# Kernel tuning notes

Measured on AMD Instinct MI355X. Metric: run time of the kernel, lower is better.

Reference implementation:

```python
import jax, jax.numpy as jnp
import numpy as np

D_MODEL = 1024
N_HEADS = 16
ALPHA = 0.7
C_PARAM = 5
CUTOFF = C_PARAM // 2 + 1  # 3
LN_EPS = 1e-12
B, S = 4, 2048


def setup_inputs() -> dict:
    key = jax.random.key(0)
    ks = jax.random.split(key, 10)
    d = D_MODEL
    scale = 1.0 / np.sqrt(d)
    return {
        "input_tensor": jax.random.normal(ks[0], (B, S, d), dtype=jnp.float32),
        "attention_mask": jnp.ones((1, 1, S, S), dtype=jnp.int32),
        "sqrt_beta": jax.random.normal(ks[1], (1, 1, d), dtype=jnp.float32),
        "ln_gamma": jnp.ones((d,), dtype=jnp.float32),
        "ln_beta": jnp.zeros((d,), dtype=jnp.float32),
        "q_w": jax.random.normal(ks[2], (d, d), dtype=jnp.float32) * scale,
        "q_b": jnp.zeros((d,), dtype=jnp.float32),
        "k_w": jax.random.normal(ks[3], (d, d), dtype=jnp.float32) * scale,
        "k_b": jnp.zeros((d,), dtype=jnp.float32),
        "v_w": jax.random.normal(ks[4], (d, d), dtype=jnp.float32) * scale,
        "v_b": jnp.zeros((d,), dtype=jnp.float32),
    }


def _layer_norm(x, g, b):
    mu = jnp.mean(x, axis=-1, keepdims=True)
    var = jnp.mean(jnp.square(x - mu), axis=-1, keepdims=True)
    return (x - mu) * jax.lax.rsqrt(var + LN_EPS) * g + b


def bsarec_layer(x, mask, sqrt_beta, ln_gamma, ln_beta, q_w, q_b, k_w, k_b, v_w, v_b):
    batch, seq_len, hidden = x.shape
    # ---- FrequencyLayer (DSP branch) ----
    xf = jnp.fft.rfft(x, axis=1, norm='ortho')                 # [B, S//2+1, D]
    freq = jnp.arange(xf.shape[1])[None, :, None]
    low_pass = jnp.fft.irfft(jnp.where(freq < CUTOFF, xf, 0.0), n=seq_len, axis=1, norm='ortho')
    high_pass = x - low_pass
    seq_fft = low_pass + jnp.square(sqrt_beta) * high_pass
    dsp = _layer_norm(seq_fft + x, ln_gamma, ln_beta)          # dropout=0 -> identity
    # ---- MultiHeadAttention (GSP branch) ----
    h, d_k = N_HEADS, hidden // N_HEADS
    def split(t):  # [B,S,D] -> [B,H,S,d_k]
        return t.reshape(batch, seq_len, h, d_k).transpose(0, 2, 1, 3)
    q = split(x @ q_w.T + q_b)
    k = split(x @ k_w.T + k_b)
    v = split(x @ v_w.T + v_b)
    scores = jnp.einsum('bhsd,bhtd->bhst', q, k) / jnp.sqrt(jnp.float32(d_k))
    scores = jnp.where(mask == 0, -jnp.inf, scores)
    scores = scores - jnp.max(scores)                           # global max, as in source
    p = jax.nn.softmax(scores, axis=-1)
    p = jnp.where(jnp.isnan(p), 0.0, p)
    out = jnp.einsum('bhst,bhtd->bhsd', p, v)
    gsp = out.transpose(0, 2, 1, 3).reshape(batch, seq_len, hidden)
    return ALPHA * dsp + (1.0 - ALPHA) * gsp


def reference(input_tensor, attention_mask, sqrt_beta, ln_gamma, ln_beta, q_w, q_b, k_w, k_b, v_w, v_b):
    return bsarec_layer(input_tensor, attention_mask, sqrt_beta, ln_gamma, ln_beta,
                        q_w, q_b, k_w, k_b, v_w, v_b)
```

## Files before the change

kernel.cpp:

```cpp
#include <hip/hip_runtime.h>

#define S_LEN 2048
#define DM 1024
#define NB 4
#define NROWS (NB * S_LEN)
#define NHEADS 16
#define DK 64

typedef __bf16 bf16x8 __attribute__((ext_vector_type(8)));
typedef __bf16 bf16x2 __attribute__((ext_vector_type(2)));
typedef float f32x4 __attribute__((ext_vector_type(4)));
typedef float f32x2 __attribute__((ext_vector_type(2)));

struct __align__(8) us4 { unsigned short x, y, z, w; };

__device__ __forceinline__ unsigned cvt2(float a, float b) {
    f32x2 t; t.x = a; t.y = b;
    bf16x2 h = __builtin_convertvector(t, bf16x2);
    return __builtin_bit_cast(unsigned, h);
}
__device__ __forceinline__ unsigned short f2bf(float f) {
    __bf16 h = (__bf16)f;
    return __builtin_bit_cast(unsigned short, h);
}

__device__ __forceinline__ void gl2lds16(const void* g, void* l) {
    __builtin_amdgcn_global_load_lds(
        (const __attribute__((address_space(1))) unsigned int*)g,
        (__attribute__((address_space(3))) unsigned int*)l, 16, 0, 0);
}

__device__ __forceinline__ void bar_lgkm() {
    __builtin_amdgcn_s_waitcnt(0xC07F);
    __builtin_amdgcn_s_barrier();
}

__global__ __launch_bounds__(256) void prep(
    const float* __restrict__ x, float* __restrict__ coef,
    unsigned short* __restrict__ xbf, const float* __restrict__ qw,
    const float* __restrict__ kw, const float* __restrict__ vw,
    unsigned short* __restrict__ wbf) {
    int bx = blockIdx.x;
    if (bx >= 512) {
        int idx = ((bx - 512) * 256 + threadIdx.x) * 2;
        int which = idx >> 20, off = idx & 0xFFFFF;
        const float* src = (which == 0) ? qw : ((which == 1) ? kw : vw);
        float2 v = *(const float2*)(&src[off]);
        *(unsigned*)(&wbf[idx]) = cvt2(v.x, v.y);
        return;
    }
    int b = bx >> 7, dc = (bx >> 5) & 3, tc = bx & 31;
    int d = dc * 256 + threadIdx.x;
    __shared__ float tw[4][64];
    if (threadIdx.x < 64) {
        const float omega = 6.283185307179586476925f / (float)S_LEN;
        float sn, cs;
        __sincosf(omega * (float)(tc * 64 + threadIdx.x), &sn, &cs);
        tw[0][threadIdx.x] = sn;
        tw[1][threadIdx.x] = cs;
        tw[2][threadIdx.x] = 2.f * sn * cs;
        tw[3][threadIdx.x] = cs * cs - sn * sn;
    }
    __syncthreads();
    float c0 = 0.f, c1 = 0.f, s1 = 0.f, c2 = 0.f, s2 = 0.f;
    for (int i = 0; i < 64; ++i) {
        int t = tc * 64 + i;
        long idx = (long)(b * S_LEN + t) * DM + d;
        float v = x[idx];
        xbf[idx] = f2bf(v);
        c0 += v;
        c1 += v * tw[1][i];
        s1 += v * tw[0][i];
        c2 += v * tw[3][i];
        s2 += v * tw[2][i];
    }
    int base = b * DM + d;
    atomicAdd(&coef[0 * 4096 + base], c0);
    atomicAdd(&coef[1 * 4096 + base], c1);
    atomicAdd(&coef[2 * 4096 + base], s1);
    atomicAdd(&coef[3 * 4096 + base], c2);
    atomicAdd(&coef[4 * 4096 + base], s2);
}

__global__ __launch_bounds__(256) void dsp_ln(
    const float* __restrict__ x, const float* __restrict__ coef,
    const float* __restrict__ sqrt_beta, const float* __restrict__ gamma,
    const float* __restrict__ beta, const unsigned short* __restrict__ Og,
    float* __restrict__ out) {
    int row = blockIdx.x;
    int b = row >> 11, t = row & (S_LEN - 1);
    int tid = threadIdx.x, lane = tid & 63, wave = tid >> 6;
    const float omega = 6.283185307179586476925f / (float)S_LEN;
    float sn, cs;
    __sincosf(omega * (float)t, &sn, &cs);
    float c2t = cs * cs - sn * sn, s2t = 2.f * sn * cs;
    int d0 = tid * 4;
    long base = (long)row * DM;
    float4 xv = *(const float4*)(&x[base + d0]);
    int cb = b * DM + d0;
    float4 C0 = *(const float4*)(&coef[0 * 4096 + cb]);
    float4 C1 = *(const float4*)(&coef[1 * 4096 + cb]);
    float4 S1 = *(const float4*)(&coef[2 * 4096 + cb]);
    float4 C2 = *(const float4*)(&coef[3 * 4096 + cb]);
    float4 S2 = *(const float4*)(&coef[4 * 4096 + cb]);
    float4 sb = *(const float4*)(&sqrt_beta[d0]);
    const float inv_s = 1.0f / (float)S_LEN;
    float y[4];
#pragma unroll
    for (int i = 0; i < 4; ++i) {
        float c0 = (&C0.x)[i], c1 = (&C1.x)[i], s1 = (&S1.x)[i],
              c2 = (&C2.x)[i], s2 = (&S2.x)[i];
        float lp = (c0 + 2.f * (c1 * cs + s1 * sn) + 2.f * (c2 * c2t + s2 * s2t)) * inv_s;
        float xx = (&xv.x)[i];
        float b2 = (&sb.x)[i];
        b2 = b2 * b2;
        y[i] = xx + lp + b2 * (xx - lp);
    }
    float ssum = y[0] + y[1] + y[2] + y[3];
    float ssq = y[0] * y[0] + y[1] * y[1] + y[2] * y[2] + y[3] * y[3];
#pragma unroll
    for (int m = 1; m < 64; m <<= 1) {
        ssum += __shfl_xor(ssum, m, 64);
        ssq += __shfl_xor(ssq, m, 64);
    }
    __shared__ float red[8];
    if (lane == 0) { red[wave] = ssum; red[4 + wave] = ssq; }
    __syncthreads();
    float S = red[0] + red[1] + red[2] + red[3];
    float SQ = red[4] + red[5] + red[6] + red[7];
    float mu = S * (1.0f / DM);
    float var = SQ * (1.0f / DM) - mu * mu;
    float rstd = rsqrtf(var + 1e-12f);
    float4 g = *(const float4*)(&gamma[d0]);
    float4 be = *(const float4*)(&beta[d0]);
    us4 gv = *(const us4*)(&Og[((long)((b << 4) + (d0 >> 6)) * S_LEN + t) * DK + (d0 & 63)]);
    const unsigned short* gp = (const unsigned short*)&gv;
    float4 o;
#pragma unroll
    for (int i = 0; i < 4; ++i)
        (&o.x)[i] = 0.7f * ((y[i] - mu) * rstd * (&g.x)[i] + (&be.x)[i]) +
                    0.3f * __uint_as_float((unsigned)gp[i] << 16);
    *(float4*)(&out[base + d0]) = o;
}

__global__ __launch_bounds__(256) void gemm_qkv(
    const unsigned short* __restrict__ A, const unsigned short* __restrict__ W,
    const float* __restrict__ qb, const float* __restrict__ kb,
    const float* __restrict__ vb, unsigned short* __restrict__ Qo,
    unsigned short* __restrict__ Ko, unsigned short* __restrict__ Vt_g) {
    const int m0 = blockIdx.y * 128;
    const int n0g = blockIdx.x * 128;
    const int which = n0g >> 10;
    const int n0 = n0g & 1023;
    const int tid = threadIdx.x;
    const int lane = tid & 63, wave = tid >> 6;
    const int wm = wave >> 1, wn = wave & 1;
    const int r = lane & 15, q = lane >> 4;
    __shared__ __align__(16) unsigned short Sm[8192];
    unsigned short* As = Sm;
    unsigned short* Bs = Sm + 4096;
    const int lrow = lane >> 2;
    const int lch = (lane & 3) * 8;
    f32x4 acc[4][4] = {};
    for (int k0 = 0; k0 < DM; k0 += 32) {
        __syncthreads();
#pragma unroll
        for (int e = 0; e < 2; ++e) {
            int blk = e * 4 + wave;
            int row = blk * 16 + lrow;
            gl2lds16(&A[(long)(m0 + row) * DM + k0 + lch], &As[blk * 512 + lane * 8]);
            gl2lds16(&W[(long)(n0g + row) * DM + k0 + lch], &Bs[blk * 512 + lane * 8]);
        }
        __syncthreads();
        bf16x8 af[4], bfr[4];
#pragma unroll
        for (int i = 0; i < 4; ++i) {
            af[i] = *(const bf16x8*)(&As[(wm * 64 + i * 16 + r) * 32 + q * 8]);
            bfr[i] = *(const bf16x8*)(&Bs[(wn * 64 + i * 16 + r) * 32 + q * 8]);
        }
#pragma unroll
        for (int mi = 0; mi < 4; ++mi)
#pragma unroll
            for (int ni = 0; ni < 4; ++ni)
                acc[mi][ni] = __builtin_amdgcn_mfma_f32_16x16x32_bf16(
                    af[mi], bfr[ni], acc[mi][ni], 0, 0, 0);
    }
    const float* bias = (which == 0) ? qb : ((which == 1) ? kb : vb);
    if (which < 2) {
        unsigned short* Out = (which == 0) ? Qo : Ko;
#pragma unroll
        for (int p = 0; p < 4; ++p) {
            __syncthreads();
            if (wm == (p >> 1)) {
#pragma unroll
                for (int mi2 = 0; mi2 < 2; ++mi2) {
                    int mi = (p & 1) * 2 + mi2;
                    int rowL = mi2 * 16 + q * 4;
#pragma unroll
                    for (int ni = 0; ni < 4; ++ni) {
                        int col = wn * 64 + ni * 16 + r;
                        float bv = bias[n0 + col];
#pragma unroll
                        for (int reg = 0; reg < 4; ++reg)
                            Sm[(rowL + reg) * 134 + col] = f2bf(acc[mi][ni][reg] + bv);
                    }
                }
            }
            __syncthreads();
            int rowL = wave * 8 + (lane >> 3);
            int cc = (lane & 7) * 16;
            uint4 w0 = *(const uint4*)(&Sm[rowL * 134 + cc]);
            uint4 w1 = *(const uint4*)(&Sm[rowL * 134 + cc + 8]);
            long gb = (long)(m0 + p * 32 + rowL) * DM + n0 + cc;
            *(uint4*)(&Out[gb]) = w0;
            *(uint4*)(&Out[gb + 8]) = w1;
        }
    } else {
        const int bb = m0 >> 11, sg = m0 & (S_LEN - 1);
#pragma unroll
        for (int p = 0; p < 4; ++p) {
            __syncthreads();
            if (wn == (p >> 1)) {
#pragma unroll
                for (int ni2 = 0; ni2 < 2; ++ni2) {
                    int ni = (p & 1) * 2 + ni2;
                    int colL = ni2 * 16 + r;
                    float bv = bias[n0 + p * 32 + colL];
#pragma unroll
                    for (int mi = 0; mi < 4; ++mi) {
                        int s = wm * 64 + mi * 16 + q * 4;
                        *(unsigned*)(&Sm[colL * 134 + s]) =
                            cvt2(acc[mi][ni][0] + bv, acc[mi][ni][1] + bv);
                        *(unsigned*)(&Sm[colL * 134 + s + 2]) =
                            cvt2(acc[mi][ni][2] + bv, acc[mi][ni][3] + bv);
                    }
                }
            }
            __syncthreads();
            int colL = wave * 8 + (lane >> 3);
            int sc = (lane & 7) * 16;
            uint4 w0 = *(const uint4*)(&Sm[colL * 134 + sc]);
            uint4 w1 = *(const uint4*)(&Sm[colL * 134 + sc + 8]);
            long gb = ((long)bb * DM + n0 + p * 32 + colL) * S_LEN + sg + sc;
            *(uint4*)(&Vt_g[gb]) = w0;
            *(uint4*)(&Vt_g[gb + 8]) = w1;
        }
    }
}

__global__ __launch_bounds__(256, 2) void attn(
    const unsigned short* __restrict__ Q, const unsigned short* __restrict__ K,
    const unsigned short* __restrict__ Vt_g, unsigned short* __restrict__ Og) {
    int bx = blockIdx.x;
    int bh = bx & 63, qt = bx >> 6;
    int b = bh >> 4, h = bh & 15;
    const int tid = threadIdx.x, lane = tid & 63, wave = tid >> 6;
    const int r = lane & 15, q = lane >> 4;
    const int hc = h * DK;
    const int q0 = qt * 256 + wave * 64;
    bf16x8 aq[4][2];
#pragma unroll
    for (int mt = 0; mt < 4; ++mt) {
        long rowQ = (long)(b * S_LEN + q0 + mt * 16 + r) * DM + hc;
        aq[mt][0] = *(const bf16x8*)(&Q[rowQ + q * 8]);
        aq[mt][1] = *(const bf16x8*)(&Q[rowQ + 32 + q * 8]);
    }
    __shared__ __align__(16) unsigned short Ks[2][64 * 72];
    __shared__ __align__(16) unsigned short Vt[2][64 * 72];
    __shared__ __align__(16) unsigned short Ps[4 * 64 * 40];
    __shared__ float denL[4 * 64];
    f32x4 accO[4][4] = {};
    float den[4] = {};
    const int srow = tid >> 3;
    const int sch = (tid & 7) * 8;
    const long kbase = (long)b * S_LEN * DM + hc + sch;
    const long vbase = ((long)bh * DK + srow) * S_LEN + sch;
    int4 kreg[2], vreg[2];
#pragma unroll
    for (int e = 0; e < 2; ++e) {
        kreg[e] = *(const int4*)(&K[kbase + (long)(e * 32 + srow) * DM]);
        vreg[e] = *(const int4*)(&Vt_g[vbase + (long)e * 32 * S_LEN]);
    }
#pragma unroll
    for (int e = 0; e < 2; ++e) {
        int rw = e * 32 + srow;
        *(int4*)(&Ks[0][rw * 72 + sch]) = kreg[e];
        *(int4*)(&Vt[0][rw * 72 + sch]) = vreg[e];
    }
    bar_lgkm();
    for (int t = 0; t < 32; ++t) {
        const unsigned short* Kc = Ks[t & 1];
        const unsigned short* Vc = Vt[t & 1];
        if (t < 31) {
            int jn = (t + 1) * 64;
#pragma unroll
            for (int e = 0; e < 2; ++e) {
                kreg[e] = *(const int4*)(&K[kbase + (long)(jn + e * 32 + srow) * DM]);
                vreg[e] = *(const int4*)(&Vt_g[vbase + (long)e * 32 * S_LEN + jn]);
            }
        }
#pragma unroll
        for (int c = 0; c < 2; ++c) {
#pragma unroll
            for (int jt2 = 0; jt2 < 2; ++jt2) {
                int jt = c * 2 + jt2;
                bf16x8 ak0 = *(const bf16x8*)(&Kc[(jt * 16 + r) * 72 + q * 8]);
                bf16x8 ak1 = *(const bf16x8*)(&Kc[(jt * 16 + r) * 72 + 32 + q * 8]);
#pragma unroll
                for (int mt = 0; mt < 4; ++mt) {
                    f32x4 s = {};
                    s = __builtin_amdgcn_mfma_f32_16x16x32_bf16(ak0, aq[mt][0], s, 0, 0, 0);
                    s = __builtin_amdgcn_mfma_f32_16x16x32_bf16(ak1, aq[mt][1], s, 0, 0, 0);
                    float p0 = __expf(s[0] * 0.125f);
                    float p1 = __expf(s[1] * 0.125f);
                    float p2 = __expf(s[2] * 0.125f);
                    float p3 = __expf(s[3] * 0.125f);
                    den[mt] += (p0 + p1) + (p2 + p3);
                    us4 pk;
                    pk.x = f2bf(p0); pk.y = f2bf(p1);
                    pk.z = f2bf(p2); pk.w = f2bf(p3);
                    *(us4*)(&Ps[(wave * 64 + mt * 16 + r) * 40 + jt2 * 16 + q * 4]) = pk;
                }
            }
            bf16x8 ap[4];
#pragma unroll
            for (int mt = 0; mt < 4; ++mt)
                ap[mt] = *(const bf16x8*)(&Ps[(wave * 64 + mt * 16 + r) * 40 + q * 8]);
#pragma unroll
            for (int dt = 0; dt < 4; ++dt) {
                bf16x8 bv = *(const bf16x8*)(&Vc[(dt * 16 + r) * 72 + c * 32 + q * 8]);
#pragma unroll
                for (int mt = 0; mt < 4; ++mt)
                    accO[mt][dt] = __builtin_amdgcn_mfma_f32_16x16x32_bf16(
                        ap[mt], bv, accO[mt][dt], 0, 0, 0);
            }
        }
        if (t < 31) {
#pragma unroll
            for (int e = 0; e < 2; ++e) {
                int rw = e * 32 + srow;
                *(int4*)(&Ks[(t + 1) & 1][rw * 72 + sch]) = kreg[e];
                *(int4*)(&Vt[(t + 1) & 1][rw * 72 + sch]) = vreg[e];
            }
        }
        bar_lgkm();
    }
#pragma unroll
    for (int mt = 0; mt < 4; ++mt) {
        float d = den[mt];
        d += __shfl_xor(d, 16, 64);
        d += __shfl_xor(d, 32, 64);
        if (q == 0) denL[wave * 64 + mt * 16 + r] = d;
    }
#pragma unroll
    for (int mt = 0; mt < 4; ++mt) {
        float4 dv = *(const float4*)(&denL[wave * 64 + mt * 16 + q * 4]);
        float rs[4];
#pragma unroll
        for (int reg = 0; reg < 4; ++reg) rs[reg] = 1.0f / (&dv.x)[reg];
        long obase = (long)bh * S_LEN + q0 + mt * 16 + q * 4;
#pragma unroll
        for (int dt = 0; dt < 4; ++dt) {
            int col = dt * 16 + r;
#pragma unroll
            for (int reg = 0; reg < 4; ++reg)
                Og[(obase + reg) * DK + col] = f2bf(accO[mt][dt][reg] * rs[reg]);
        }
    }
}

extern "C" void kernel_launch(void* const* d_in, const int* in_sizes, int n_in,
                              void* d_out, int out_size, void* d_ws, size_t ws_size,
                              hipStream_t stream) {
    const float* x = (const float*)d_in[0];
    const float* sqrt_beta = (const float*)d_in[2];
    const float* gamma = (const float*)d_in[3];
    const float* beta = (const float*)d_in[4];
    const float* qw = (const float*)d_in[5];
    const float* qb = (const float*)d_in[6];
    const float* kw = (const float*)d_in[7];
    const float* kb = (const float*)d_in[8];
    const float* vw = (const float*)d_in[9];
    const float* vb = (const float*)d_in[10];
    float* out = (float*)d_out;

    char* ws = (char*)d_ws;
    float* coef = (float*)ws;
    unsigned short* xbf = (unsigned short*)(ws + 81920);
    unsigned short* wbf = (unsigned short*)(ws + 81920 + 16777216);
    unsigned short* Qb = (unsigned short*)(ws + 81920 + 16777216 + 6291456);
    unsigned short* Kb = Qb + (long)NROWS * DM;
    unsigned short* Vt_g = Kb + (long)NROWS * DM;
    unsigned short* Og = xbf;

    hipMemsetAsync(coef, 0, 5 * 4096 * sizeof(float), stream);
    prep<<<6656, 256, 0, stream>>>(x, coef, xbf, qw, kw, vw, wbf);
    dim3 ggrid(3 * DM / 128, NROWS / 128);
    gemm_qkv<<<ggrid, 256, 0, stream>>>(xbf, wbf, qb, kb, vb, Qb, Kb, Vt_g);
    attn<<<NB * NHEADS * (S_LEN / 256), 256, 0, stream>>>(Qb, Kb, Vt_g, Og);
    dsp_ln<<<NROWS, 256, 0, stream>>>(x, coef, sqrt_beta, gamma, beta, Og, out);
}
```

Baseline: 304.9 us.

## Restructure attention: register-resident P, async LDS loads, exp2 prescaled Q, smaller tiles

The attention kernel now keeps softmax probabilities in registers and feeds them straight into the PV MFMA, which removes the Ps shared-memory round trip. K and V tiles are loaded with global_load_lds directly into swizzled, unpadded LDS. The softmax scale and log2(e) are folded into Q in the GEMM epilogue so exp2 can replace expf. The query tile per block is halved to 128 rows, which doubles the grid and raises the occupancy target to 3 blocks per CU. In exchange the kernel relies on subtle swizzle index math and on the bf16 rounding of the scaled Q.

```diff
diff --git a/kernel.cpp b/kernel.cpp
--- a/kernel.cpp
+++ b/kernel.cpp
@@ -11,6 +11,7 @@
 typedef __bf16 bf16x2 __attribute__((ext_vector_type(2)));
 typedef float f32x4 __attribute__((ext_vector_type(4)));
 typedef float f32x2 __attribute__((ext_vector_type(2)));
+typedef unsigned u32x4 __attribute__((ext_vector_type(4)));
 
 struct __align__(8) us4 { unsigned short x, y, z, w; };
 
@@ -30,10 +31,11 @@
         (__attribute__((address_space(3))) unsigned int*)l, 16, 0, 0);
 }
 
-__device__ __forceinline__ void bar_lgkm() {
-    __builtin_amdgcn_s_waitcnt(0xC07F);
-    __builtin_amdgcn_s_barrier();
-}
+#if __has_builtin(__builtin_amdgcn_exp2f)
+#define EXP2F(x) __builtin_amdgcn_exp2f(x)
+#else
+#define EXP2F(x) exp2f(x)
+#endif
 
 __global__ __launch_bounds__(256) void prep(
     const float* __restrict__ x, float* __restrict__ coef,
@@ -187,6 +189,7 @@
     }
     const float* bias = (which == 0) ? qb : ((which == 1) ? kb : vb);
     if (which < 2) {
+        const float qs = (which == 0) ? 0.18033688011112042f : 1.0f;
         unsigned short* Out = (which == 0) ? Qo : Ko;
 #pragma unroll
         for (int p = 0; p < 4; ++p) {
@@ -202,7 +205,7 @@
                         float bv = bias[n0 + col];
 #pragma unroll
                         for (int reg = 0; reg < 4; ++reg)
-                            Sm[(rowL + reg) * 134 + col] = f2bf(acc[mi][ni][reg] + bv);
+                            Sm[(rowL + reg) * 134 + col] = f2bf((acc[mi][ni][reg] + bv) * qs);
                     }
                 }
             }
@@ -248,7 +251,7 @@
     }
 }
 
-__global__ __launch_bounds__(256, 2) void attn(
+__global__ __launch_bounds__(256, 3) void attn(
     const unsigned short* __restrict__ Q, const unsigned short* __restrict__ K,
     const unsigned short* __restrict__ Vt_g, unsigned short* __restrict__ Og) {
     int bx = blockIdx.x;
@@ -257,104 +260,113 @@
     const int tid = threadIdx.x, lane = tid & 63, wave = tid >> 6;
     const int r = lane & 15, q = lane >> 4;
     const int hc = h * DK;
-    const int q0 = qt * 256 + wave * 64;
-    bf16x8 aq[4][2];
-#pragma unroll
-    for (int mt = 0; mt < 4; ++mt) {
+    const int q0 = qt * 128 + wave * 32;
+
+    bf16x8 aq[2][2];
+#pragma unroll
+    for (int mt = 0; mt < 2; ++mt) {
         long rowQ = (long)(b * S_LEN + q0 + mt * 16 + r) * DM + hc;
         aq[mt][0] = *(const bf16x8*)(&Q[rowQ + q * 8]);
         aq[mt][1] = *(const bf16x8*)(&Q[rowQ + 32 + q * 8]);
     }
-    __shared__ __align__(16) unsigned short Ks[2][64 * 72];
-    __shared__ __align__(16) unsigned short Vt[2][64 * 72];
-    __shared__ __align__(16) unsigned short Ps[4 * 64 * 40];
-    __shared__ float denL[4 * 64];
-    f32x4 accO[4][4] = {};
-    float den[4] = {};
-    const int srow = tid >> 3;
-    const int sch = (tid & 7) * 8;
-    const long kbase = (long)b * S_LEN * DM + hc + sch;
-    const long vbase = ((long)bh * DK + srow) * S_LEN + sch;
-    int4 kreg[2], vreg[2];
-#pragma unroll
-    for (int e = 0; e < 2; ++e) {
-        kreg[e] = *(const int4*)(&K[kbase + (long)(e * 32 + srow) * DM]);
-        vreg[e] = *(const int4*)(&Vt_g[vbase + (long)e * 32 * S_LEN]);
-    }
-#pragma unroll
-    for (int e = 0; e < 2; ++e) {
-        int rw = e * 32 + srow;
-        *(int4*)(&Ks[0][rw * 72 + sch]) = kreg[e];
-        *(int4*)(&Vt[0][rw * 72 + sch]) = vreg[e];
-    }
-    bar_lgkm();
+
+    __shared__ __align__(16) unsigned short Ks[2][4096];
+    __shared__ __align__(16) unsigned short Vt[2][4096];
+    __shared__ float denL[128];
+
+    f32x4 accO[2][4] = {};
+    float den[2] = {};
+
+    const int lr = lane >> 3, lc = lane & 7;
+    const int cw0 = wave * 2, cw1 = cw0 + 1;
+    const int ld0 = cw0 * 512, ld1 = cw1 * 512;
+    const int row0 = cw0 * 8 + lr, row1 = cw1 * 8 + lr;
+    const int f0 = (lr + 2 * (cw0 & 3)) & 7;
+    const int f1 = (lr + 2 * (cw1 & 3)) & 7;
+    const int cg0 = (lc - f0) & 7, cg1 = (lc - f1) & 7;
+    const unsigned short* kp0 = K + (long)(b * S_LEN + row0) * DM + hc + cg0 * 8;
+    const unsigned short* kp1 = K + (long)(b * S_LEN + row1) * DM + hc + cg1 * 8;
+    const unsigned short* vp0 = Vt_g + (long)(bh * 64 + row0) * S_LEN + cg0 * 8;
+    const unsigned short* vp1 = Vt_g + (long)(bh * 64 + row1) * S_LEN + cg1 * 8;
+
+    const int lo = r & 3, hi = r >> 2;
+    const int abase = (hi * 8 + lo) * 64;
+    const int e0 = (q + lo + 2 * hi) & 7;
+    const int ca = e0 * 8;
+    const int cb2 = ((e0 + 4) & 7) * 8;
+    const int fv = ((r & 7) + 2 * (r >> 3)) & 7;
+    const int vca = ((q + fv) & 7) * 8;
+    const int vcb = ((q + fv + 4) & 7) * 8;
+
+    gl2lds16(kp0, &Ks[0][ld0 + lane * 8]);
+    gl2lds16(kp1, &Ks[0][ld1 + lane * 8]);
+    gl2lds16(vp0, &Vt[0][ld0 + lane * 8]);
+    gl2lds16(vp1, &Vt[0][ld1 + lane * 8]);
+    kp0 += 64 * DM; kp1 += 64 * DM; vp0 += 64; vp1 += 64;
+    asm volatile("s_waitcnt vmcnt(0)" ::: "memory");
+    __builtin_amdgcn_s_barrier();
+
     for (int t = 0; t < 32; ++t) {
-        const unsigned short* Kc = Ks[t & 1];
-        const unsigned short* Vc = Vt[t & 1];
+        const int cur = t & 1;
         if (t < 31) {
-            int jn = (t + 1) * 64;
-#pragma unroll
-            for (int e = 0; e < 2; ++e) {
-                kreg[e] = *(const int4*)(&K[kbase + (long)(jn + e * 32 + srow) * DM]);
-                vreg[e] = *(const int4*)(&Vt_g[vbase + (long)e * 32 * S_LEN + jn]);
+            const int nb = cur ^ 1;
+            gl2lds16(kp0, &Ks[nb][ld0 + lane * 8]);
+            gl2lds16(kp1, &Ks[nb][ld1 + lane * 8]);
+            gl2lds16(vp0, &Vt[nb][ld0 + lane * 8]);
+            gl2lds16(vp1, &Vt[nb][ld1 + lane * 8]);
+            kp0 += 64 * DM; kp1 += 64 * DM; vp0 += 64; vp1 += 64;
+        }
+        const unsigned short* Kc = Ks[cur];
+        const unsigned short* Vc = Vt[cur];
+#pragma unroll
+        for (int c = 0; c < 2; ++c) {
+            const int cb64 = c * 2048;
+            bf16x8 ak00 = *(const bf16x8*)(&Kc[cb64 + abase + ca]);
+            bf16x8 ak01 = *(const bf16x8*)(&Kc[cb64 + abase + cb2]);
+            bf16x8 ak10 = *(const bf16x8*)(&Kc[cb64 + 256 + abase + cb2]);
+            bf16x8 ak11 = *(const bf16x8*)(&Kc[cb64 + 256 + abase + ca]);
+            const int va = c ? vcb : vca;
+            const int vb2 = c ? vca : vcb;
+            bf16x8 bv[4];
+            bv[0] = *(const bf16x8*)(&Vc[(0 * 16 + r) * 64 + va]);
+            bv[1] = *(const bf16x8*)(&Vc[(1 * 16 + r) * 64 + vb2]);
+            bv[2] = *(const bf16x8*)(&Vc[(2 * 16 + r) * 64 + va]);
+            bv[3] = *(const bf16x8*)(&Vc[(3 * 16 + r) * 64 + vb2]);
+#pragma unroll
+            for (int mt = 0; mt < 2; ++mt) {
+                f32x4 sa = {}, sb = {};
+                sa = __builtin_amdgcn_mfma_f32_16x16x32_bf16(ak00, aq[mt][0], sa, 0, 0, 0);
+                sa = __builtin_amdgcn_mfma_f32_16x16x32_bf16(ak01, aq[mt][1], sa, 0, 0, 0);
+                sb = __builtin_amdgcn_mfma_f32_16x16x32_bf16(ak10, aq[mt][0], sb, 0, 0, 0);
+                sb = __builtin_amdgcn_mfma_f32_16x16x32_bf16(ak11, aq[mt][1], sb, 0, 0, 0);
+                float p0 = EXP2F(sa[0]), p1 = EXP2F(sa[1]);
+                float p2 = EXP2F(sa[2]), p3 = EXP2F(sa[3]);
+                float p4 = EXP2F(sb[0]), p5 = EXP2F(sb[1]);
+                float p6 = EXP2F(sb[2]), p7 = EXP2F(sb[3]);
+                den[mt] += ((p0 + p1) + (p2 + p3)) + ((p4 + p5) + (p6 + p7));
+                u32x4 wv;
+                wv.x = cvt2(p0, p1); wv.y = cvt2(p2, p3);
+                wv.z = cvt2(p4, p5); wv.w = cvt2(p6, p7);
+                bf16x8 ap = __builtin_bit_cast(bf16x8, wv);
+#pragma unroll
+                for (int dt = 0; dt < 4; ++dt)
+                    accO[mt][dt] = __builtin_amdgcn_mfma_f32_16x16x32_bf16(
+                        ap, bv[dt], accO[mt][dt], 0, 0, 0);
             }
         }
-#pragma unroll
-        for (int c = 0; c < 2; ++c) {
-#pragma unroll
-            for (int jt2 = 0; jt2 < 2; ++jt2) {
-                int jt = c * 2 + jt2;
-                bf16x8 ak0 = *(const bf16x8*)(&Kc[(jt * 16 + r) * 72 + q * 8]);
-                bf16x8 ak1 = *(const bf16x8*)(&Kc[(jt * 16 + r) * 72 + 32 + q * 8]);
-#pragma unroll
-                for (int mt = 0; mt < 4; ++mt) {
-                    f32x4 s = {};
-                    s = __builtin_amdgcn_mfma_f32_16x16x32_bf16(ak0, aq[mt][0], s, 0, 0, 0);
-                    s = __builtin_amdgcn_mfma_f32_16x16x32_bf16(ak1, aq[mt][1], s, 0, 0, 0);
-                    float p0 = __expf(s[0] * 0.125f);
-                    float p1 = __expf(s[1] * 0.125f);
-                    float p2 = __expf(s[2] * 0.125f);
-                    float p3 = __expf(s[3] * 0.125f);
-                    den[mt] += (p0 + p1) + (p2 + p3);
-                    us4 pk;
-                    pk.x = f2bf(p0); pk.y = f2bf(p1);
-                    pk.z = f2bf(p2); pk.w = f2bf(p3);
-                    *(us4*)(&Ps[(wave * 64 + mt * 16 + r) * 40 + jt2 * 16 + q * 4]) = pk;
-                }
-            }
-            bf16x8 ap[4];
-#pragma unroll
-            for (int mt = 0; mt < 4; ++mt)
-                ap[mt] = *(const bf16x8*)(&Ps[(wave * 64 + mt * 16 + r) * 40 + q * 8]);
-#pragma unroll
-            for (int dt = 0; dt < 4; ++dt) {
-                bf16x8 bv = *(const bf16x8*)(&Vc[(dt * 16 + r) * 72 + c * 32 + q * 8]);
-#pragma unroll
-                for (int mt = 0; mt < 4; ++mt)
-                    accO[mt][dt] = __builtin_amdgcn_mfma_f32_16x16x32_bf16(
-                        ap[mt], bv, accO[mt][dt], 0, 0, 0);
-            }
-        }
-        if (t < 31) {
-#pragma unroll
-            for (int e = 0; e < 2; ++e) {
-                int rw = e * 32 + srow;
-                *(int4*)(&Ks[(t + 1) & 1][rw * 72 + sch]) = kreg[e];
-                *(int4*)(&Vt[(t + 1) & 1][rw * 72 + sch]) = vreg[e];
-            }
-        }
-        bar_lgkm();
-    }
-#pragma unroll
-    for (int mt = 0; mt < 4; ++mt) {
+        asm volatile("s_waitcnt vmcnt(0)" ::: "memory");
+        __builtin_amdgcn_s_barrier();
+    }
+#pragma unroll
+    for (int mt = 0; mt < 2; ++mt) {
         float d = den[mt];
         d += __shfl_xor(d, 16, 64);
         d += __shfl_xor(d, 32, 64);
-        if (q == 0) denL[wave * 64 + mt * 16 + r] = d;
-    }
-#pragma unroll
-    for (int mt = 0; mt < 4; ++mt) {
-        float4 dv = *(const float4*)(&denL[wave * 64 + mt * 16 + q * 4]);
+        if (q == 0) denL[wave * 32 + mt * 16 + r] = d;
+    }
+#pragma unroll
+    for (int mt = 0; mt < 2; ++mt) {
+        float4 dv = *(const float4*)(&denL[wave * 32 + mt * 16 + q * 4]);
         float rs[4];
 #pragma unroll
         for (int reg = 0; reg < 4; ++reg) rs[reg] = 1.0f / (&dv.x)[reg];
@@ -397,6 +409,6 @@
     prep<<<6656, 256, 0, stream>>>(x, coef, xbf, qw, kw, vw, wbf);
     dim3 ggrid(3 * DM / 128, NROWS / 128);
     gemm_qkv<<<ggrid, 256, 0, stream>>>(xbf, wbf, qb, kb, vb, Qb, Kb, Vt_g);
-    attn<<<NB * NHEADS * (S_LEN / 256), 256, 0, stream>>>(Qb, Kb, Vt_g, Og);
+    attn<<<NB * NHEADS * (S_LEN / 128), 256, 0, stream>>>(Qb, Kb, Vt_g, Og);
     dsp_ln<<<NROWS, 256, 0, stream>>>(x, coef, sqrt_beta, gamma, beta, Og, out);
 }
```

New measurement: 300.9 us. No clear change (-1.3%).
